# Kernel tuning notes

Measured on AMD Instinct MI355X. Metric: run time of the kernel, lower is better.

The kernel has to match this reference:

```python
import jax, jax.numpy as jnp
import numpy as np

EPS = 1e-5

def avg_pool3s2(x):
    # AvgPool2d(kernel=3, stride=2, no padding) on NCHW
    s = jax.lax.reduce_window(x, 0.0, jax.lax.add, (1, 1, 3, 3), (1, 1, 2, 2), 'VALID')
    return s / 9.0

def conv1x1(x, W):
    # x: [n,c,h,w], W: [out,c]
    return jnp.einsum('nchw,oc->nohw', x, W)

def batchnorm(x, g, b):
    # training-mode BN over (N,H,W), biased variance (matches torch normalization)
    m = x.mean(axis=(0, 2, 3), keepdims=True)
    v = x.var(axis=(0, 2, 3), keepdims=True)
    return (x - m) * jax.lax.rsqrt(v + EPS) * g[None, :, None, None] + b[None, :, None, None]

def coord_features(hp, wp):
    # [8, hp, wp]: xmin, ymin, xmax, ymax, xctr, yctr, 1/W, 1/H
    w = jnp.arange(wp, dtype=jnp.float32)
    h = jnp.arange(hp, dtype=jnp.float32)
    xmin = w / wp * 2 - 1
    xmax = (w + 1) / wp * 2 - 1
    xctr = (xmin + xmax) / 2
    ymin = h / hp * 2 - 1
    ymax = (h + 1) / hp * 2 - 1
    yctr = (ymin + ymax) / 2
    bx = lambda a: jnp.broadcast_to(a[None, :], (hp, wp))
    by = lambda a: jnp.broadcast_to(a[:, None], (hp, wp))
    const = lambda v: jnp.full((hp, wp), v, dtype=jnp.float32)
    return jnp.stack([bx(xmin), by(ymin), bx(xmax), by(ymax), bx(xctr), by(yctr),
                      const(1.0 / wp), const(1.0 / hp)], axis=0)

def resize_bilinear_ac(x, H, W):
    # bilinear upsample with align_corners=True, x: [n,c,h,w]
    h, w = x.shape[2], x.shape[3]
    ys = jnp.linspace(0.0, h - 1.0, H)
    xs = jnp.linspace(0.0, w - 1.0, W)
    y0 = jnp.floor(ys).astype(jnp.int32); y1 = jnp.minimum(y0 + 1, h - 1); wy = (ys - y0)[None, None, :, None]
    x0 = jnp.floor(xs).astype(jnp.int32); x1 = jnp.minimum(x0 + 1, w - 1); wx = (xs - x0)[None, None, None, :]
    rows = x[:, :, y0, :] * (1 - wy) + x[:, :, y1, :] * wy          # [n,c,H,w]
    return rows[:, :, :, x0] * (1 - wx) + rows[:, :, :, x1] * wx    # [n,c,H,W]

def setup_inputs() -> dict:
    key = jax.random.key(0)
    ks = jax.random.split(key, 8)
    n, in_dim, hid, h, w = 4, 256, 10, 129, 129
    d = hid + 8  # 18
    return {
        'p_fea': jax.random.normal(ks[0], (n, in_dim, h, w), dtype=jnp.float32),
        'hu': jax.random.normal(ks[1], (n, hid, h, w), dtype=jnp.float32),
        'Wq': jax.random.normal(ks[2], (d, d), dtype=jnp.float32) * 0.05,
        'Wk': jax.random.normal(ks[3], (d, in_dim + 8), dtype=jnp.float32) * 0.05,
        'Wv': jax.random.normal(ks[4], (128, in_dim), dtype=jnp.float32) * 0.05,
        'g_v': jnp.ones((128,), dtype=jnp.float32),
        'b_v': jnp.zeros((128,), dtype=jnp.float32),
        'Wp': jax.random.normal(ks[5], (hid, 128), dtype=jnp.float32) * 0.05,
        'g_p': jnp.ones((hid,), dtype=jnp.float32),
        'b_p': jnp.zeros((hid,), dtype=jnp.float32),
    }

def reference(p_fea, hu, Wq, Wk, Wv, g_v, b_v, Wp, g_p, b_p):
    n, c, h, w = p_fea.shape
    p = avg_pool3s2(p_fea)   # [n,256,hp,wp]
    u = avg_pool3s2(hu)      # [n,10,hp,wp]
    hp, wp = p.shape[2], p.shape[3]
    L = hp * wp
    coord = jnp.broadcast_to(coord_features(hp, wp)[None], (n, 8, hp, wp))
    query = conv1x1(jnp.concatenate([u, coord], axis=1), Wq).reshape(n, -1, L).transpose(0, 2, 1)  # [n,L,18]
    key_t = conv1x1(jnp.concatenate([p, coord], axis=1), Wk).reshape(n, -1, L)                      # [n,18,L]
    val = jax.nn.relu(batchnorm(conv1x1(p, Wv), g_v, b_v)).reshape(n, 128, L)                       # [n,128,L]
    energy = jnp.einsum('nlc,ncm->nlm', query, key_t)            # [n,L,L]
    attn = jax.nn.softmax(energy, axis=-1)
    ctx = jnp.einsum('ncm,nlm->ncl', val, attn).reshape(n, 128, hp, wp)
    ctx = jax.nn.relu(batchnorm(conv1x1(ctx, Wp), g_p, b_p))     # [n,10,hp,wp]
    return resize_bilinear_ac(ctx, h, w)                          # [n,10,h,w]
```

## Files before the change

kernel.cpp:

```cpp
#include <hip/hip_runtime.h>
#include <hip/hip_bf16.h>
#include <cstdint>

#define NN   4
#define LL   4096
#define DD   18
#define CVV  128
#define CIN  256
#define CUU  10
#define HH   129
#define COO  10

typedef unsigned short ushort_t;
typedef __attribute__((ext_vector_type(8))) short short8v;
typedef __attribute__((ext_vector_type(4))) float f32x4;

#define PT_OFF   ((size_t)0)
#define OP_OFF   ((size_t)2097152)
#define VAL_OFF  ((size_t)2260992)
#define QT_OFF   ((size_t)3309568)
#define KT_OFF   ((size_t)3571712)
#define VT_OFF   ((size_t)3833856)
#define VSC_OFF  ((size_t)4882432)
#define VSH_OFF  ((size_t)4882560)
#define S2_OFF   ((size_t)4882688)
#define SH2_OFF  ((size_t)4882704)
#define PART_OFF ((size_t)4882720)
#define PART2_OFF ((size_t)4948256)
#define KMAX_OFF ((size_t)4949536)

#define LOG2E 1.44269504088896f

static __device__ __forceinline__ ushort_t f2bf(float x) {
    unsigned int u = __float_as_uint(x);
    unsigned int r = (u + 0x7fffu + ((u >> 16) & 1u)) >> 16;
    return (ushort_t)r;
}
static __device__ __forceinline__ float bf2f(ushort_t b) {
    return __uint_as_float(((unsigned int)b) << 16);
}
static __device__ __forceinline__ float exp2_hw(float x) {
    float r;
    asm("v_exp_f32 %0, %1" : "=v"(r) : "v"(x));
    return r;
}
static __device__ __forceinline__ unsigned int cvtpk(float lo, float hi) {
    unsigned int r;
    asm("v_cvt_pk_bf16_f32 %0, %1, %2" : "=v"(r) : "v"(lo), "v"(hi));
    return r;
}

static __device__ __forceinline__ void gload16(const void* g, void* l) {
    __builtin_amdgcn_global_load_lds(
        (const __attribute__((address_space(1))) void*)g,
        (__attribute__((address_space(3))) void*)l, 16, 0, 0);
}

__global__ __launch_bounds__(256) void pool_pt_kernel(const float* __restrict__ src,
                                                      ushort_t* __restrict__ pt,
                                                      int* __restrict__ kz) {
    if (kz != nullptr && blockIdx.x == 0 && threadIdx.x < 128) kz[threadIdx.x] = 0;
    int b = blockIdx.x;
    int rg = b & 15;
    int cg = (b >> 4) & 31;
    int n  = b >> 9;

    __shared__ float rows[8][9][132];
    const float* base = src + ((size_t)(n * CIN + cg * 8)) * (HH * HH) + (size_t)(rg * 8) * HH;
    #pragma unroll
    for (int rr = 0; rr < 9; ++rr) {
        for (int t = threadIdx.x; t < 264; t += 256) {
            int ch = t / 33;
            int c4 = t - ch * 33;
            const float* rp = base + (size_t)ch * (HH * HH) + (size_t)rr * HH;
            if (c4 < 32) {
                float4 v = *(const float4*)(rp + c4 * 4);
                *(float4*)&rows[ch][rr][c4 * 4] = v;
            } else {
                rows[ch][rr][128] = rp[128];
            }
        }
    }
    __syncthreads();

    int row = threadIdx.x >> 6, ow = threadIdx.x & 63;
    int x = 2 * ow;
    union { short8v v; ushort_t s[8]; } pk;
    #pragma unroll
    for (int ch = 0; ch < 8; ++ch) {
        const float* r0 = rows[ch][2 * row];
        const float* r1 = rows[ch][2 * row + 1];
        const float* r2 = rows[ch][2 * row + 2];
        float sum = r0[x] + r0[x + 1] + r0[x + 2]
                  + r1[x] + r1[x + 1] + r1[x + 2]
                  + r2[x] + r2[x + 1] + r2[x + 2];
        pk.s[ch] = f2bf(sum * (1.0f / 9.0f));
    }
    int m = (rg * 4 + row) * 64 + ow;
    *(short8v*)(pt + (((size_t)(n * 32 + cg)) * 4096 + m) * 8) = pk.v;
}

__global__ __launch_bounds__(256, 2) void qkval4_kernel(const ushort_t* __restrict__ pt,
                                                        const float* __restrict__ hu,
                                                        const float* __restrict__ Wq,
                                                        const float* __restrict__ Wk,
                                                        const float* __restrict__ Wv,
                                                        ushort_t* __restrict__ qt,
                                                        char* __restrict__ kt_c,
                                                        int* __restrict__ kmaxb,
                                                        ushort_t* __restrict__ val,
                                                        float* __restrict__ part) {
    __shared__ __align__(16) char smem[39936];
    int tid = threadIdx.x;
    int bmod = blockIdx.x % 3;

    if (bmod != 2) {
        float (*WkL)[DD] = (float(*)[DD])smem;
        float (*kacc)[32][21] = (float(*)[32][21])(smem + 18432);
        int bq = (blockIdx.x / 3) * 2 + bmod;
        int n  = bq >> 7;
        int mb = bq & 127;
        int w = tid >> 6;
        int lane = tid & 63;
        int mloc = lane & 31;
        int chh = lane >> 5;
        int m = mb * 32 + mloc;
        int hi = m >> 6, wi = m & 63;

        for (int e = tid; e < CIN * DD; e += 256) {
            int cc = e / DD, o = e - (e / DD) * DD;
            WkL[cc][o] = Wk[o * 264 + cc];
        }
        __syncthreads();

        float coord[8];
        coord[0] = wi * (2.0f / 64.0f) - 1.0f;
        coord[1] = hi * (2.0f / 64.0f) - 1.0f;
        coord[2] = (wi + 1) * (2.0f / 64.0f) - 1.0f;
        coord[3] = (hi + 1) * (2.0f / 64.0f) - 1.0f;
        coord[4] = 0.5f * (coord[0] + coord[2]);
        coord[5] = 0.5f * (coord[1] + coord[3]);
        coord[6] = 1.0f / 64.0f;
        coord[7] = 1.0f / 64.0f;

        {
            float acc[DD];
            #pragma unroll
            for (int o = 0; o < DD; ++o) acc[o] = 0.0f;
            #pragma unroll
            for (int j = 0; j < 4; ++j) {
                int cgi = w * 8 + chh * 4 + j;
                union { short8v v; ushort_t s[8]; } ps;
                ps.v = *(const short8v*)(pt + (((size_t)(n * 32 + cgi)) * 4096 + m) * 8);
                #pragma unroll
                for (int i = 0; i < 8; ++i) {
                    float pv = bf2f(ps.s[i]);
                    const float* wr = WkL[cgi * 8 + i];
                    #pragma unroll
                    for (int o = 0; o < DD; ++o) acc[o] = fmaf(pv, wr[o], acc[o]);
                }
            }
            if (w == 3 && chh == 1) {
                #pragma unroll
                for (int j = 0; j < 8; ++j) {
                    float cv = coord[j];
                    #pragma unroll
                    for (int o = 0; o < DD; ++o) acc[o] = fmaf(cv, Wk[o * 264 + CIN + j], acc[o]);
                }
            }
            #pragma unroll
            for (int o = 0; o < DD; ++o) kacc[w * 2 + chh][mloc][o] = acc[o];
        }
        if (w == 0 && chh == 0) {
            float acc[DD];
            #pragma unroll
            for (int o = 0; o < DD; ++o) acc[o] = 0.0f;
            const float* hub = hu + ((size_t)(n * CUU)) * (HH * HH) + (size_t)(2 * hi) * HH + 2 * wi;
            for (int cq = 0; cq < CUU; ++cq) {
                const float* s = hub + (size_t)cq * (HH * HH);
                float uv = (s[0] + s[1] + s[2]
                          + s[HH] + s[HH + 1] + s[HH + 2]
                          + s[2 * HH] + s[2 * HH + 1] + s[2 * HH + 2]) * (1.0f / 9.0f);
                #pragma unroll
                for (int o = 0; o < DD; ++o) acc[o] = fmaf(uv, Wq[o * DD + cq], acc[o]);
            }
            #pragma unroll
            for (int j = 0; j < 8; ++j) {
                float cv = coord[j];
                #pragma unroll
                for (int o = 0; o < DD; ++o) acc[o] = fmaf(cv, Wq[o * DD + CUU + j], acc[o]);
            }
            union { short8v v[4]; ushort_t s[32]; } pk;
            #pragma unroll
            for (int o = 0; o < 32; ++o) pk.s[o] = (o < DD) ? f2bf(acc[o] * LOG2E) : (ushort_t)0;
            short8v* qrow = (short8v*)(qt + ((size_t)(n * LL) + m) * 32);
            #pragma unroll
            for (int j = 0; j < 4; ++j) qrow[j] = pk.v[j];
        }
        __syncthreads();
        if (tid < 128) {
            int j = tid >> 5;
            int mloc2 = tid & 31;
            int m2 = mb * 32 + mloc2;
            union { short8v v; ushort_t s[8]; } pk;
            #pragma unroll
            for (int i = 0; i < 8; ++i) {
                int o = j * 8 + i;
                float v = 0.0f;
                if (o < DD) {
                    v = kacc[0][mloc2][o] + kacc[1][mloc2][o] + kacc[2][mloc2][o] + kacc[3][mloc2][o]
                      + kacc[4][mloc2][o] + kacc[5][mloc2][o] + kacc[6][mloc2][o] + kacc[7][mloc2][o];
                }
                pk.s[i] = (o < DD) ? f2bf(v) : (ushort_t)0;
            }
            int ktile = m2 >> 6;
            int m64 = m2 & 63;
            int byte = ((m64 << 6) | (j << 4)) ^ (((m64 >> 1) & 7) << 4);
            *(short8v*)(kt_c + (size_t)n * 262144 + (size_t)ktile * 4096 + byte) = pk.v;

            int mb8[8];
            #pragma unroll
            for (int i = 0; i < 8; ++i) mb8[i] = (int)(pk.s[i] & 0x7fffu);
            #pragma unroll
            for (int off = 1; off < 32; off <<= 1) {
                #pragma unroll
                for (int i = 0; i < 8; ++i) {
                    int ov = __shfl_xor(mb8[i], off);
                    mb8[i] = max(mb8[i], ov);
                }
            }
            if (mloc2 == 0) {
                #pragma unroll
                for (int i = 0; i < 8; ++i)
                    atomicMax(&kmaxb[n * 32 + j * 8 + i], mb8[i] << 16);
            }
        }
    } else {
        int b2 = blockIdx.x / 3;
        int n  = b2 >> 6;
        int mb = b2 & 63;
        int m0 = mb * 64;
        int w = tid >> 6, lane = tid & 63, cl = lane & 15, g = lane >> 4;

        f32x4 acc[2][4];
        #pragma unroll
        for (int t = 0; t < 2; ++t)
            #pragma unroll
            for (int mt = 0; mt < 4; ++mt) acc[t][mt] = (f32x4){0.f, 0.f, 0.f, 0.f};

        #pragma unroll 2
        for (int kc = 0; kc < 8; ++kc) {
            short8v bfr[4];
            const ushort_t* pb2 = pt + (((size_t)(n * 32 + kc * 4 + g)) * 4096) * 8;
            #pragma unroll
            for (int mt = 0; mt < 4; ++mt)
                bfr[mt] = *(const short8v*)(pb2 + (size_t)(m0 + mt * 16 + cl) * 8);
            #pragma unroll
            for (int t = 0; t < 2; ++t) {
                int ch = (2 * w + t) * 16 + cl;
                const float* wr = Wv + (size_t)ch * CIN + kc * 32 + 8 * g;
                float4 wa = *(const float4*)wr;
                float4 wb = *(const float4*)(wr + 4);
                union { short8v v; ushort_t s[8]; } af;
                af.s[0] = f2bf(wa.x); af.s[1] = f2bf(wa.y); af.s[2] = f2bf(wa.z); af.s[3] = f2bf(wa.w);
                af.s[4] = f2bf(wb.x); af.s[5] = f2bf(wb.y); af.s[6] = f2bf(wb.z); af.s[7] = f2bf(wb.w);
                #pragma unroll
                for (int mt = 0; mt < 4; ++mt)
                    acc[t][mt] = __builtin_amdgcn_mfma_f32_16x16x32_bf16(af.v, bfr[mt], acc[t][mt], 0, 0, 0);
            }
        }

        #pragma unroll
        for (int t = 0; t < 2; ++t) {
            float s1[4] = {0.f, 0.f, 0.f, 0.f}, s2[4] = {0.f, 0.f, 0.f, 0.f};
            #pragma unroll
            for (int mt = 0; mt < 4; ++mt) {
                #pragma unroll
                for (int r = 0; r < 4; ++r) {
                    float v = acc[t][mt][r];
                    s1[r] += v;
                    s2[r] = fmaf(v, v, s2[r]);
                    int ch = (2 * w + t) * 16 + g * 4 + r;
                    val[((size_t)(n * CVV + ch)) * LL + m0 + mt * 16 + cl] = f2bf(v);
                }
            }
            #pragma unroll
            for (int off = 1; off < 16; off <<= 1) {
                #pragma unroll
                for (int r = 0; r < 4; ++r) {
                    s1[r] += __shfl_xor(s1[r], off);
                    s2[r] += __shfl_xor(s2[r], off);
                }
            }
            if (cl == 0) {
                #pragma unroll
                for (int r = 0; r < 4; ++r) {
                    int ch = (2 * w + t) * 16 + g * 4 + r;
                    size_t idx = (((size_t)b2) * CVV + ch) * 2;
                    part[idx]     = s1[r];
                    part[idx + 1] = s2[r];
                }
            }
        }
    }
}

__global__ __launch_bounds__(128) void bn_finalize_v2_kernel(const float* __restrict__ part,
                                                             const float* __restrict__ g,
                                                             const float* __restrict__ bta,
                                                             float* __restrict__ scale,
                                                             float* __restrict__ shift) {
    int ch = threadIdx.x;
    if (ch >= CVV) return;
    float s1 = 0.0f, s2 = 0.0f;
    for (int b = 0; b < 256; ++b) {
        size_t idx = ((size_t)b * CVV + ch) * 2;
        s1 += part[idx];
        s2 += part[idx + 1];
    }
    float mean = s1 * (1.0f / (NN * LL));
    float var = s2 * (1.0f / (NN * LL)) - mean * mean;
    float inv = rsqrtf(var + 1e-5f);
    float sc = g[ch] * inv;
    scale[ch] = sc;
    shift[ch] = bta[ch] - mean * sc;
}

__global__ __launch_bounds__(256) void bn_apply2_kernel(const ushort_t* __restrict__ val,
                                                        const float* __restrict__ scale,
                                                        const float* __restrict__ shift,
                                                        char* __restrict__ vt_c) {
    int t = blockIdx.x * 256 + threadIdx.x;
    int mq = t & 511;
    int ch = (t >> 9) & 127;
    int n = t >> 16;
    int m0 = mq * 8;
    short8v vs = *(const short8v*)(val + ((size_t)(n * CVV + ch)) * LL + m0);
    float sc = scale[ch], sh = shift[ch];
    union { short8v v; ushort_t s[8]; } pk;
    #pragma unroll
    for (int i = 0; i < 8; ++i)
        pk.s[i] = f2bf(fmaxf(fmaf(bf2f((ushort_t)vs[i]), sc, sh), 0.0f));
    int tile = m0 >> 5, mloc = m0 & 31;
    size_t byte = (size_t)n * 1048576 + (size_t)tile * 8192
                + (size_t)(((ch << 6) | (mloc << 1)) ^ ((ch & 7) << 4));
    *(short8v*)(vt_c + byte) = pk.v;
}

__global__ __launch_bounds__(256, 4) void attn_swz_kernel(const ushort_t* __restrict__ qt,
                                                          const char* __restrict__ kt_c,
                                                          const char* __restrict__ vt_c,
                                                          const int* __restrict__ kmaxb,
                                                          const float* __restrict__ Wp,
                                                          float* __restrict__ ypart,
                                                          float* __restrict__ Lp) {
    int orig = blockIdx.x;
    int xcd = orig & 7;
    int idx = orig >> 3;
    int qb = idx >> 1;
    int combo = xcd * 2 + (idx & 1);
    int n = combo >> 2;
    int sM = combo & 3;
    int T0 = sM * 32;

    int tid = threadIdx.x;
    int w = tid >> 6, lane = tid & 63, c = lane & 15, g = lane >> 4;
    int l0w = qb * 64 + w * 16;

    __shared__ __align__(16) ushort_t K_t[2][1024];
    __shared__ __align__(16) ushort_t V_t[2][4096];
    __shared__ __align__(16) uint4 exch[4][64];
    __shared__ float Wpl[COO][CVV];

    for (int i = tid; i < COO * CVV; i += 256) Wpl[i >> 7][i & 127] = Wp[i];

    const char* ktb = kt_c + (size_t)n * 262144;
    const char* vtb = vt_c + (size_t)n * 1048576;

    short8v qf = *(const short8v*)(qt + (((size_t)n * LL + l0w + c) << 5) + g * 8);
    int vxor = (c & 7) << 4;

    float Mq = 0.0f;
    {
        const int* km = kmaxb + n * 32 + g * 8;
        #pragma unroll
        for (int i = 0; i < 8; ++i) {
            float kv = __int_as_float(km[i]);
            float aq = __uint_as_float(((unsigned int)((ushort_t)qf[i]) & 0x7fffu) << 16);
            Mq = fmaf(aq, kv, Mq);
        }
        Mq += __shfl_xor(Mq, 16);
        Mq += __shfl_xor(Mq, 32);
    }

    f32x4 O[8];
    #pragma unroll
    for (int i = 0; i < 8; ++i) O[i] = (f32x4){0.f, 0.f, 0.f, 0.f};
    float Lacc = 0.0f;

    int kby0, kby1;
    {
        int kr0 = c, kr1 = 16 + c;
        kby0 = ((kr0 << 6) | (g << 4)) ^ (((kr0 >> 1) & 7) << 4);
        kby1 = ((kr1 << 6) | (g << 4)) ^ (((kr1 >> 1) & 7) << 4);
    }
    int srcA = ((g & 1) << 5) + c;
    int toff = (g >> 1) * 8;

    {
        int T = T0;
        const char* ks = ktb + (size_t)(T >> 1) * 4096 + (T & 1) * 2048 + w * 1024 + lane * 16;
        if (w < 2) gload16(ks, (char*)K_t[0] + w * 1024);
        const char* vs = vtb + (size_t)T * 8192 + w * 2048 + lane * 16;
        gload16(vs, (char*)V_t[0] + w * 2048);
        gload16(vs + 1024, (char*)V_t[0] + w * 2048 + 1024);
    }
    __syncthreads();
    int buf = 0;
    for (int mt = 0; mt < 32; ++mt) {
        if (mt + 1 < 32) {
            int T = T0 + mt + 1;
            const char* ks = ktb + (size_t)(T >> 1) * 4096 + (T & 1) * 2048 + w * 1024 + lane * 16;
            if (w < 2) gload16(ks, (char*)K_t[buf ^ 1] + w * 1024);
            const char* vs = vtb + (size_t)T * 8192 + w * 2048 + lane * 16;
            gload16(vs, (char*)V_t[buf ^ 1] + w * 2048);
            gload16(vs + 1024, (char*)V_t[buf ^ 1] + w * 2048 + 1024);
        }
        const char* kb = (const char*)K_t[buf];
        short8v kf0 = *(const short8v*)(kb + kby0);
        short8v kf1 = *(const short8v*)(kb + kby1);
        f32x4 S0 = __builtin_amdgcn_mfma_f32_16x16x32_bf16(kf0, qf, (f32x4){0.f,0.f,0.f,0.f}, 0, 0, 0);
        f32x4 S1 = __builtin_amdgcn_mfma_f32_16x16x32_bf16(kf1, qf, (f32x4){0.f,0.f,0.f,0.f}, 0, 0, 0);
        float p0[4], p1[4];
        #pragma unroll
        for (int r = 0; r < 4; ++r) {
            p0[r] = exp2_hw(S0[r] - Mq);
            p1[r] = exp2_hw(S1[r] - Mq);
            Lacc += p0[r] + p1[r];
        }
        exch[w][lane] = (uint4){ cvtpk(p0[0], p0[1]), cvtpk(p0[2], p0[3]),
                                 cvtpk(p1[0], p1[1]), cvtpk(p1[2], p1[3]) };
        const char* eb = (const char*)&exch[w][0];
        uint2 ua = *(const uint2*)(eb + srcA * 16 + toff);
        uint2 ub = *(const uint2*)(eb + (srcA + 16) * 16 + toff);
        union { unsigned int u[4]; short8v v; } pa;
        pa.u[0] = ua.x; pa.u[1] = ua.y; pa.u[2] = ub.x; pa.u[3] = ub.y;
        const char* vb = (const char*)V_t[buf];
        __builtin_amdgcn_s_setprio(1);
        #pragma unroll
        for (int ct = 0; ct < 8; ++ct) {
            int vby = (((ct * 16 + c) << 6) | (g << 4)) ^ vxor;
            short8v vf = *(const short8v*)(vb + vby);
            O[ct] = __builtin_amdgcn_mfma_f32_16x16x32_bf16(pa.v, vf, O[ct], 0, 0, 0);
        }
        __builtin_amdgcn_s_setprio(0);
        __syncthreads();
        buf ^= 1;
    }
    Lacc += __shfl_xor(Lacc, 16);
    Lacc += __shfl_xor(Lacc, 32);
    if (g == 0)
        Lp[sM * (NN * LL) + n * LL + l0w + c] = Lacc;

    float yp[COO][4];
    #pragma unroll
    for (int o = 0; o < COO; ++o)
        #pragma unroll
        for (int r = 0; r < 4; ++r) yp[o][r] = 0.0f;
    #pragma unroll
    for (int ct = 0; ct < 8; ++ct) {
        #pragma unroll
        for (int o = 0; o < COO; ++o) {
            float wv = Wpl[o][ct * 16 + c];
            #pragma unroll
            for (int r = 0; r < 4; ++r)
                yp[o][r] = fmaf(O[ct][r], wv, yp[o][r]);
        }
    }
    #pragma unroll
    for (int off = 1; off < 16; off <<= 1) {
        #pragma unroll
        for (int o = 0; o < COO; ++o)
            #pragma unroll
            for (int r = 0; r < 4; ++r)
                yp[o][r] += __shfl_xor(yp[o][r], off);
    }
    if (c == 0) {
        #pragma unroll
        for (int r = 0; r < 4; ++r) {
            size_t yrow = (size_t)(sM * (NN * LL) + n * LL + l0w + g * 4 + r);
            #pragma unroll
            for (int o = 0; o < COO; ++o)
                ypart[yrow * COO + o] = yp[o][r];
        }
    }
}

__global__ __launch_bounds__(256) void combine4b_kernel(const float* __restrict__ ypart,
                                                        const float* __restrict__ Lp,
                                                        float* __restrict__ out_pre,
                                                        float* __restrict__ part2) {
    int idx = blockIdx.x * 256 + threadIdx.x;
    int n = idx >> 12;
    int l = idx & 4095;
    int nl = n * LL + l;
    float inv = 1.0f / (Lp[nl] + Lp[16384 + nl] + Lp[2 * 16384 + nl] + Lp[3 * 16384 + nl]);
    const float* y0 = ypart + (size_t)nl * COO;
    const float* y1 = ypart + ((size_t)16384 + nl) * COO;
    const float* y2 = ypart + ((size_t)(2 * 16384) + nl) * COO;
    const float* y3 = ypart + ((size_t)(3 * 16384) + nl) * COO;
    float ov[COO];
    #pragma unroll
    for (int o = 0; o < COO; ++o) {
        ov[o] = (y0[o] + y1[o] + y2[o] + y3[o]) * inv;
        out_pre[((size_t)(n * COO + o)) * LL + l] = ov[o];
    }
    float p1[COO], p2[COO];
    #pragma unroll
    for (int o = 0; o < COO; ++o) { p1[o] = ov[o]; p2[o] = ov[o] * ov[o]; }
    #pragma unroll
    for (int off = 1; off < 64; off <<= 1) {
        #pragma unroll
        for (int o = 0; o < COO; ++o) {
            p1[o] += __shfl_xor(p1[o], off);
            p2[o] += __shfl_xor(p2[o], off);
        }
    }
    __shared__ float rs1[4][COO], rs2[4][COO];
    int w = threadIdx.x >> 6, lane = threadIdx.x & 63;
    if (lane == 0) {
        #pragma unroll
        for (int o = 0; o < COO; ++o) { rs1[w][o] = p1[o]; rs2[w][o] = p2[o]; }
    }
    __syncthreads();
    if (threadIdx.x < COO) {
        int o = threadIdx.x;
        float a = rs1[0][o] + rs1[1][o] + rs1[2][o] + rs1[3][o];
        float b = rs2[0][o] + rs2[1][o] + rs2[2][o] + rs2[3][o];
        part2[((size_t)blockIdx.x * COO + o) * 2]     = a;
        part2[((size_t)blockIdx.x * COO + o) * 2 + 1] = b;
    }
}

__global__ __launch_bounds__(64) void bn_finalize2_kernel(const float* __restrict__ part2,
                                                          const float* __restrict__ g,
                                                          const float* __restrict__ bta,
                                                          float* __restrict__ scale,
                                                          float* __restrict__ shift) {
    int ch = threadIdx.x;
    if (ch >= COO) return;
    float s1 = 0.0f, s2 = 0.0f;
    for (int b = 0; b < 64; ++b) {
        s1 += part2[((size_t)b * COO + ch) * 2];
        s2 += part2[((size_t)b * COO + ch) * 2 + 1];
    }
    float mean = s1 * (1.0f / (NN * LL));
    float var = s2 * (1.0f / (NN * LL)) - mean * mean;
    float inv = rsqrtf(var + 1e-5f);
    float sc = g[ch] * inv;
    scale[ch] = sc;
    shift[ch] = bta[ch] - mean * sc;
}

__global__ __launch_bounds__(256) void resize_kernel(const float* __restrict__ out_pre,
                                                     const float* __restrict__ scale,
                                                     const float* __restrict__ shift,
                                                     float* __restrict__ out,
                                                     int total) {
    int idx = blockIdx.x * 256 + threadIdx.x;
    if (idx >= total) return;
    int ow = idx % HH;
    int t = idx / HH;
    int oh = t % HH;
    int t2 = t / HH;
    int o = t2 % COO;
    int n = t2 / COO;

    const float r = 63.0f / 128.0f;
    float y = oh * r;
    float x = ow * r;
    int y0 = (int)y;
    int x0 = (int)x;
    float wy = y - y0;
    float wx = x - x0;
    int y1 = min(y0 + 1, 63);
    int x1 = min(x0 + 1, 63);

    const float* base = out_pre + ((size_t)(n * COO + o)) * LL;
    float sc = scale[o], sh = shift[o];
    float v00 = fmaxf(fmaf(base[y0 * 64 + x0], sc, sh), 0.0f);
    float v01 = fmaxf(fmaf(base[y0 * 64 + x1], sc, sh), 0.0f);
    float v10 = fmaxf(fmaf(base[y1 * 64 + x0], sc, sh), 0.0f);
    float v11 = fmaxf(fmaf(base[y1 * 64 + x1], sc, sh), 0.0f);
    float top = v00 * (1.0f - wx) + v01 * wx;
    float bot = v10 * (1.0f - wx) + v11 * wx;
    out[idx] = top * (1.0f - wy) + bot * wy;
}

extern "C" void kernel_launch(void* const* d_in, const int* in_sizes, int n_in,
                              void* d_out, int out_size, void* d_ws, size_t ws_size,
                              hipStream_t stream) {
    (void)in_sizes; (void)n_in; (void)out_size; (void)ws_size;
    const float* p_fea = (const float*)d_in[0];
    const float* hu    = (const float*)d_in[1];
    const float* Wq    = (const float*)d_in[2];
    const float* Wk    = (const float*)d_in[3];
    const float* Wv    = (const float*)d_in[4];
    const float* g_v   = (const float*)d_in[5];
    const float* b_v   = (const float*)d_in[6];
    const float* Wp    = (const float*)d_in[7];
    const float* g_p   = (const float*)d_in[8];
    const float* b_p   = (const float*)d_in[9];

    float* ws = (float*)d_ws;
    ushort_t* ptb     = (ushort_t*)(ws + PT_OFF);
    float*    out_pre = ws + OP_OFF;
    ushort_t* valb    = (ushort_t*)(ws + VAL_OFF);
    ushort_t* qtb     = (ushort_t*)(ws + QT_OFF);
    char*     ktb     = (char*)(ws + KT_OFF);
    char*     vtb     = (char*)(ws + VT_OFF);
    float*    Lpart   = ws + VAL_OFF;
    float*    ypart   = ws + VAL_OFF + 65536;
    float*    vscale  = ws + VSC_OFF;
    float*    vshift  = ws + VSH_OFF;
    float*    scale2  = ws + S2_OFF;
    float*    shift2  = ws + SH2_OFF;
    float*    part    = ws + PART_OFF;
    float*    part2   = ws + PART2_OFF;
    int*      kmaxb   = (int*)(ws + KMAX_OFF);

    pool_pt_kernel<<<NN * 32 * 16, 256, 0, stream>>>(p_fea, ptb, kmaxb);
    qkval4_kernel<<<768, 256, 0, stream>>>(ptb, hu, Wq, Wk, Wv, qtb, ktb, kmaxb, valb, part);
    bn_finalize_v2_kernel<<<1, 128, 0, stream>>>(part, g_v, b_v, vscale, vshift);
    bn_apply2_kernel<<<(NN * CVV * 512) / 256, 256, 0, stream>>>(valb, vscale, vshift, vtb);
    attn_swz_kernel<<<1024, 256, 0, stream>>>(qtb, ktb, vtb, kmaxb, Wp, ypart, Lpart);
    combine4b_kernel<<<(NN * LL) / 256, 256, 0, stream>>>(ypart, Lpart, out_pre, part2);
    bn_finalize2_kernel<<<1, 64, 0, stream>>>(part2, g_p, b_p, scale2, shift2);
    {
        int total = NN * COO * HH * HH;
        resize_kernel<<<(total + 255) / 256, 256, 0, stream>>>(out_pre, scale2, shift2,
                                                               (float*)d_out, total);
    }
}
```

Before: 132.5 us.

## Double key tile width to 64 per iteration in attention kernel

Each loop iteration of the attention kernel now handles 64 keys instead of 32, so there are half as many iterations (16) and half as many block-wide barriers. The value tensor layout written by the BN-apply kernel changes to 64-key tiles to match. Shared memory per block roughly doubles and launch bounds drop from 4 to 3 blocks per CU, so occupancy and latency hiding may suffer. The larger step also gives more independent MFMA and exp work between barriers.

```diff
diff --git a/kernel.cpp b/kernel.cpp
--- a/kernel.cpp
+++ b/kernel.cpp
@@ -341,13 +341,13 @@
     #pragma unroll
     for (int i = 0; i < 8; ++i)
         pk.s[i] = f2bf(fmaxf(fmaf(bf2f((ushort_t)vs[i]), sc, sh), 0.0f));
-    int tile = m0 >> 5, mloc = m0 & 31;
-    size_t byte = (size_t)n * 1048576 + (size_t)tile * 8192
-                + (size_t)(((ch << 6) | (mloc << 1)) ^ ((ch & 7) << 4));
+    int tile = m0 >> 6, mloc = m0 & 63;
+    size_t byte = (size_t)n * 1048576 + (size_t)tile * 16384
+                + (size_t)(((ch << 7) | (mloc << 1)) ^ ((ch & 7) << 4));
     *(short8v*)(vt_c + byte) = pk.v;
 }
 
-__global__ __launch_bounds__(256, 4) void attn_swz_kernel(const ushort_t* __restrict__ qt,
+__global__ __launch_bounds__(256, 3) void attn_swz_kernel(const ushort_t* __restrict__ qt,
                                                           const char* __restrict__ kt_c,
                                                           const char* __restrict__ vt_c,
                                                           const int* __restrict__ kmaxb,
@@ -361,15 +361,15 @@
     int combo = xcd * 2 + (idx & 1);
     int n = combo >> 2;
     int sM = combo & 3;
-    int T0 = sM * 32;
+    int T0 = sM * 16;
 
     int tid = threadIdx.x;
     int w = tid >> 6, lane = tid & 63, c = lane & 15, g = lane >> 4;
     int l0w = qb * 64 + w * 16;
 
-    __shared__ __align__(16) ushort_t K_t[2][1024];
-    __shared__ __align__(16) ushort_t V_t[2][4096];
-    __shared__ __align__(16) uint4 exch[4][64];
+    __shared__ __align__(16) ushort_t K_t[2][2048];
+    __shared__ __align__(16) ushort_t V_t[2][8192];
+    __shared__ __align__(16) uint4 exch[4][2][64];
     __shared__ float Wpl[COO][CVV];
 
     for (int i = tid; i < COO * CVV; i += 256) Wpl[i >> 7][i & 127] = Wp[i];
@@ -398,60 +398,72 @@
     for (int i = 0; i < 8; ++i) O[i] = (f32x4){0.f, 0.f, 0.f, 0.f};
     float Lacc = 0.0f;
 
-    int kby0, kby1;
-    {
-        int kr0 = c, kr1 = 16 + c;
-        kby0 = ((kr0 << 6) | (g << 4)) ^ (((kr0 >> 1) & 7) << 4);
-        kby1 = ((kr1 << 6) | (g << 4)) ^ (((kr1 >> 1) & 7) << 4);
+    int kbyS[4];
+    #pragma unroll
+    for (int sub = 0; sub < 4; ++sub) {
+        int m64 = sub * 16 + c;
+        kbyS[sub] = ((m64 << 6) | (g << 4)) ^ (((m64 >> 1) & 7) << 4);
     }
     int srcA = ((g & 1) << 5) + c;
     int toff = (g >> 1) * 8;
 
     {
         int T = T0;
-        const char* ks = ktb + (size_t)(T >> 1) * 4096 + (T & 1) * 2048 + w * 1024 + lane * 16;
-        if (w < 2) gload16(ks, (char*)K_t[0] + w * 1024);
-        const char* vs = vtb + (size_t)T * 8192 + w * 2048 + lane * 16;
-        gload16(vs, (char*)V_t[0] + w * 2048);
-        gload16(vs + 1024, (char*)V_t[0] + w * 2048 + 1024);
+        const char* ks = ktb + (size_t)T * 4096 + w * 1024 + lane * 16;
+        gload16(ks, (char*)K_t[0] + w * 1024);
+        const char* vs = vtb + (size_t)T * 16384 + w * 4096 + lane * 16;
+        #pragma unroll
+        for (int i = 0; i < 4; ++i)
+            gload16(vs + i * 1024, (char*)V_t[0] + w * 4096 + i * 1024);
     }
     __syncthreads();
     int buf = 0;
-    for (int mt = 0; mt < 32; ++mt) {
-        if (mt + 1 < 32) {
+    for (int mt = 0; mt < 16; ++mt) {
+        if (mt + 1 < 16) {
             int T = T0 + mt + 1;
-            const char* ks = ktb + (size_t)(T >> 1) * 4096 + (T & 1) * 2048 + w * 1024 + lane * 16;
-            if (w < 2) gload16(ks, (char*)K_t[buf ^ 1] + w * 1024);
-            const char* vs = vtb + (size_t)T * 8192 + w * 2048 + lane * 16;
-            gload16(vs, (char*)V_t[buf ^ 1] + w * 2048);
-            gload16(vs + 1024, (char*)V_t[buf ^ 1] + w * 2048 + 1024);
+            const char* ks = ktb + (size_t)T * 4096 + w * 1024 + lane * 16;
+            gload16(ks, (char*)K_t[buf ^ 1] + w * 1024);
+            const char* vs = vtb + (size_t)T * 16384 + w * 4096 + lane * 16;
+            #pragma unroll
+            for (int i = 0; i < 4; ++i)
+                gload16(vs + i * 1024, (char*)V_t[buf ^ 1] + w * 4096 + i * 1024);
         }
         const char* kb = (const char*)K_t[buf];
-        short8v kf0 = *(const short8v*)(kb + kby0);
-        short8v kf1 = *(const short8v*)(kb + kby1);
-        f32x4 S0 = __builtin_amdgcn_mfma_f32_16x16x32_bf16(kf0, qf, (f32x4){0.f,0.f,0.f,0.f}, 0, 0, 0);
-        f32x4 S1 = __builtin_amdgcn_mfma_f32_16x16x32_bf16(kf1, qf, (f32x4){0.f,0.f,0.f,0.f}, 0, 0, 0);
-        float p0[4], p1[4];
+        f32x4 S0 = __builtin_amdgcn_mfma_f32_16x16x32_bf16(*(const short8v*)(kb + kbyS[0]), qf, (f32x4){0.f,0.f,0.f,0.f}, 0, 0, 0);
+        f32x4 S1 = __builtin_amdgcn_mfma_f32_16x16x32_bf16(*(const short8v*)(kb + kbyS[1]), qf, (f32x4){0.f,0.f,0.f,0.f}, 0, 0, 0);
+        f32x4 S2 = __builtin_amdgcn_mfma_f32_16x16x32_bf16(*(const short8v*)(kb + kbyS[2]), qf, (f32x4){0.f,0.f,0.f,0.f}, 0, 0, 0);
+        f32x4 S3 = __builtin_amdgcn_mfma_f32_16x16x32_bf16(*(const short8v*)(kb + kbyS[3]), qf, (f32x4){0.f,0.f,0.f,0.f}, 0, 0, 0);
+        float p0[4], p1[4], p2[4], p3[4];
         #pragma unroll
         for (int r = 0; r < 4; ++r) {
             p0[r] = exp2_hw(S0[r] - Mq);
             p1[r] = exp2_hw(S1[r] - Mq);
-            Lacc += p0[r] + p1[r];
-        }
-        exch[w][lane] = (uint4){ cvtpk(p0[0], p0[1]), cvtpk(p0[2], p0[3]),
-                                 cvtpk(p1[0], p1[1]), cvtpk(p1[2], p1[3]) };
-        const char* eb = (const char*)&exch[w][0];
-        uint2 ua = *(const uint2*)(eb + srcA * 16 + toff);
-        uint2 ub = *(const uint2*)(eb + (srcA + 16) * 16 + toff);
-        union { unsigned int u[4]; short8v v; } pa;
-        pa.u[0] = ua.x; pa.u[1] = ua.y; pa.u[2] = ub.x; pa.u[3] = ub.y;
+            p2[r] = exp2_hw(S2[r] - Mq);
+            p3[r] = exp2_hw(S3[r] - Mq);
+            Lacc += (p0[r] + p1[r]) + (p2[r] + p3[r]);
+        }
+        exch[w][0][lane] = (uint4){ cvtpk(p0[0], p0[1]), cvtpk(p0[2], p0[3]),
+                                    cvtpk(p1[0], p1[1]), cvtpk(p1[2], p1[3]) };
+        exch[w][1][lane] = (uint4){ cvtpk(p2[0], p2[1]), cvtpk(p2[2], p2[3]),
+                                    cvtpk(p3[0], p3[1]), cvtpk(p3[2], p3[3]) };
+        union { unsigned int u[4]; short8v v; } pa[2];
+        #pragma unroll
+        for (int mh = 0; mh < 2; ++mh) {
+            const char* eb = (const char*)&exch[w][mh][0];
+            uint2 ua = *(const uint2*)(eb + srcA * 16 + toff);
+            uint2 ub = *(const uint2*)(eb + (srcA + 16) * 16 + toff);
+            pa[mh].u[0] = ua.x; pa[mh].u[1] = ua.y; pa[mh].u[2] = ub.x; pa[mh].u[3] = ub.y;
+        }
         const char* vb = (const char*)V_t[buf];
         __builtin_amdgcn_s_setprio(1);
         #pragma unroll
         for (int ct = 0; ct < 8; ++ct) {
-            int vby = (((ct * 16 + c) << 6) | (g << 4)) ^ vxor;
-            short8v vf = *(const short8v*)(vb + vby);
-            O[ct] = __builtin_amdgcn_mfma_f32_16x16x32_bf16(pa.v, vf, O[ct], 0, 0, 0);
+            int vby0 = (((ct * 16 + c) << 7) | (g << 4)) ^ vxor;
+            int vby1 = (((ct * 16 + c) << 7) | 64 | (g << 4)) ^ vxor;
+            short8v vf0 = *(const short8v*)(vb + vby0);
+            short8v vf1 = *(const short8v*)(vb + vby1);
+            O[ct] = __builtin_amdgcn_mfma_f32_16x16x32_bf16(pa[0].v, vf0, O[ct], 0, 0, 0);
+            O[ct] = __builtin_amdgcn_mfma_f32_16x16x32_bf16(pa[1].v, vf1, O[ct], 0, 0, 0);
         }
         __builtin_amdgcn_s_setprio(0);
         __syncthreads();
```

After: 136.4 us. 1.03x slower.
